# Kernel optimization log

Hardware: AMD Instinct MI355X
Metric: run time of the kernel (lower is better)

Reference implementation:

```python
import jax, jax.numpy as jnp
import numpy as np

B, S, E, H = 16, 256, 4096, 16
D = E // H  # 256; module's matmul pattern requires S == D and B == H


def setup_inputs() -> dict:
    rng = jax.random.key(0)
    k0, k1, k2, k3, k4 = jax.random.split(rng, 5)
    return {
        "query": jax.random.normal(k0, (B, S, E), jnp.float32),
        "key": jax.random.normal(k1, (B, S, E), jnp.float32),
        "value": jax.random.normal(k2, (B, S, E), jnp.float32),
        # out_proj: torch nn.Linear(E, E) -> y = x @ W.T + b
        "out_w": jax.random.normal(k3, (E, E), jnp.float32) * 0.02,
        "out_b": jnp.zeros((E,), jnp.float32),
    }


def reference(query, key, value, out_w, out_b):
    scale = D ** -0.5
    # split heads: [B, S, E] -> [B, H, S, D]
    q = (query * scale).reshape(B, S, H, D).transpose(0, 2, 1, 3)
    k = key.reshape(B, S, H, D).transpose(0, 2, 1, 3)
    v = value.reshape(B, S, H, D).transpose(0, 2, 1, 3)
    # torch.matmul(q_head, k_head) with NO transpose: contracts q's D with k's S
    # (valid because S == D). aw: [B, H, S, D]
    aw = jnp.einsum('bhit,bhtj->bhij', q, k)
    # attn_weights.transpose(0, 1): [B, H, ...] -> [H, B, ...]
    aw = jnp.swapaxes(aw, 0, 1)
    # eval mode path: softmax over last dim (no dropout)
    aw = jax.nn.softmax(aw, axis=-1)
    # torch.matmul(aw [H,B,S,D], v [B,H,S,D]): batch dims broadcast because B == H,
    # pairing elementwise -> out[x,y] = aw[x,y] @ v[x,y]
    out = jnp.einsum('xyit,xytj->xyij', aw, v)
    # transpose(1, 2) then reshape to (B, S, E)
    out = jnp.swapaxes(out, 1, 2).reshape(B, S, E)
    # out_proj
    return out @ out_w.T + out_b
```

## Files before the change

### kernel.cpp

```cpp
#include <hip/hip_runtime.h>

#define AS1 __attribute__((address_space(1)))
#define AS3 __attribute__((address_space(3)))

typedef __bf16 bf16x8 __attribute__((ext_vector_type(8)));
typedef float f32x4 __attribute__((ext_vector_type(4)));

__device__ __forceinline__ unsigned short f2bf(float f) {
  unsigned int u = __builtin_bit_cast(unsigned int, f);
  u += 0x7fffu + ((u >> 16) & 1u);
  return (unsigned short)(u >> 16);
}

__global__ __launch_bounds__(256) void kv_transpose(
    const float* __restrict__ key, const float* __restrict__ value,
    unsigned short* __restrict__ KT2, unsigned short* __restrict__ VT2) {
  __shared__ float tr[32 * 33];
  const int tid = threadIdx.x;
  const int ts  = blockIdx.y;
  const int pp  = blockIdx.x >> 3;
  const int s   = blockIdx.x & 7;
  const int b   = ts ? (pp >> 4) : (pp & 15);
  const int h   = ts ? (pp & 15) : (pp >> 4);
  const float* src = (ts ? value : key) + ((size_t)(b * 256 + s * 32)) * 4096 + h * 256;
  unsigned short* dst = (ts ? VT2 : KT2) + (size_t)(pp * 8 + s) * 8192;
  const int tt = tid >> 3;
  const int q8 = tid & 7;
  for (int jb = 0; jb < 8; ++jb) {
    float4 v = *(const float4*)(src + (size_t)tt * 4096 + jb * 32 + q8 * 4);
    tr[tt * 33 + q8 * 4 + 0] = v.x;
    tr[tt * 33 + q8 * 4 + 1] = v.y;
    tr[tt * 33 + q8 * 4 + 2] = v.z;
    tr[tt * 33 + q8 * 4 + 3] = v.w;
    __syncthreads();
    ushort4 o;
    o.x = f2bf(tr[(q8 * 4 + 0) * 33 + tt]);
    o.y = f2bf(tr[(q8 * 4 + 1) * 33 + tt]);
    o.z = f2bf(tr[(q8 * 4 + 2) * 33 + tt]);
    o.w = f2bf(tr[(q8 * 4 + 3) * 33 + tt]);
    *(ushort4*)(dst + (jb * 32 + tt) * 32 + q8 * 4) = o;
    __syncthreads();
  }
}

__global__ __launch_bounds__(256, 2) void attn_kernel(
    const float* __restrict__ qin, const unsigned short* __restrict__ KT2,
    const unsigned short* __restrict__ VT2, unsigned short* __restrict__ attn) {
  __shared__ __align__(16) unsigned short kv[8192];
  __shared__ __align__(16) unsigned short plds[4 * 16 * 264];

  const int tid  = threadIdx.x;
  const int lane = tid & 63;
  const int wave = tid >> 6;
  const int li   = lane & 15;
  const int ks   = lane >> 4;

  const int bid = blockIdx.x;
  const int pp  = (bid & 7) * 32 + ((bid >> 3) & 31);
  const int ib  = bid >> 8;
  const int x = pp >> 4, y = pp & 15;
  const int i0 = ib * 64 + wave * 16;

  bf16x8 qf[8];
  {
    const float* qrow = qin + ((size_t)(y * 256 + i0 + li)) * 4096 + x * 256 + ks * 8;
#pragma unroll
    for (int s = 0; s < 8; ++s) {
      float4 v0 = *(const float4*)(qrow + s * 32);
      float4 v1 = *(const float4*)(qrow + s * 32 + 4);
      union { bf16x8 v; unsigned short u[8]; } t;
      t.u[0] = f2bf(v0.x * 0.0625f); t.u[1] = f2bf(v0.y * 0.0625f);
      t.u[2] = f2bf(v0.z * 0.0625f); t.u[3] = f2bf(v0.w * 0.0625f);
      t.u[4] = f2bf(v1.x * 0.0625f); t.u[5] = f2bf(v1.y * 0.0625f);
      t.u[6] = f2bf(v1.z * 0.0625f); t.u[7] = f2bf(v1.w * 0.0625f);
      qf[s] = t.v;
    }
  }

  const f32x4 vzero = {0.f, 0.f, 0.f, 0.f};
  f32x4 sacc[16];
#pragma unroll
  for (int f = 0; f < 16; ++f) sacc[f] = vzero;

  const unsigned short* ktile = KT2 + (size_t)pp * 65536;
#pragma unroll
  for (int s = 0; s < 8; ++s) {
    __syncthreads();
#pragma unroll
    for (int cc = 0; cc < 4; ++cc) {
      const unsigned short* g = ktile + (size_t)s * 8192 + (cc * 256 + tid) * 8;
      __builtin_amdgcn_global_load_lds((AS1 unsigned int*)g,
          (AS3 unsigned int*)((AS3 char*)kv + cc * 4096 + wave * 1024), 16, 0, 0);
    }
    __syncthreads();
#pragma unroll
    for (int f = 0; f < 16; ++f) {
      bf16x8 bfr = *(const bf16x8*)&kv[(f * 16 + li) * 32 + ks * 8];
      sacc[f] = __builtin_amdgcn_mfma_f32_16x16x32_bf16(qf[s], bfr, sacc[f], 0, 0, 0);
    }
  }

  float sm[4];
#pragma unroll
  for (int qi = 0; qi < 4; ++qi) {
    float m = sacc[0][qi];
#pragma unroll
    for (int f = 1; f < 16; ++f) m = fmaxf(m, sacc[f][qi]);
    m = fmaxf(m, __shfl_xor(m, 1));
    m = fmaxf(m, __shfl_xor(m, 2));
    m = fmaxf(m, __shfl_xor(m, 4));
    m = fmaxf(m, __shfl_xor(m, 8));
    float ssum = 0.f;
#pragma unroll
    for (int f = 0; f < 16; ++f) {
      float pv = __expf(sacc[f][qi] - m);
      sacc[f][qi] = pv;
      ssum += pv;
    }
    ssum += __shfl_xor(ssum, 1);
    ssum += __shfl_xor(ssum, 2);
    ssum += __shfl_xor(ssum, 4);
    ssum += __shfl_xor(ssum, 8);
    sm[qi] = ssum;
  }

  unsigned short* pw = plds + wave * 4224;
#pragma unroll
  for (int f = 0; f < 16; ++f)
#pragma unroll
    for (int qi = 0; qi < 4; ++qi)
      pw[(ks * 4 + qi) * 264 + f * 16 + li] = f2bf(sacc[f][qi]);

  f32x4 oacc[16];
#pragma unroll
  for (int f = 0; f < 16; ++f) oacc[f] = vzero;
  const unsigned short* vtile = VT2 + (size_t)pp * 65536;
  const unsigned short* pr = plds + wave * 4224 + li * 264;
#pragma unroll
  for (int s2 = 0; s2 < 8; ++s2) {
    __syncthreads();
#pragma unroll
    for (int cc = 0; cc < 4; ++cc) {
      const unsigned short* g = vtile + (size_t)s2 * 8192 + (cc * 256 + tid) * 8;
      __builtin_amdgcn_global_load_lds((AS1 unsigned int*)g,
          (AS3 unsigned int*)((AS3 char*)kv + cc * 4096 + wave * 1024), 16, 0, 0);
    }
    __syncthreads();
    bf16x8 afr = *(const bf16x8*)&pr[s2 * 32 + ks * 8];
#pragma unroll
    for (int f = 0; f < 16; ++f) {
      bf16x8 bfr = *(const bf16x8*)&kv[(f * 16 + li) * 32 + ks * 8];
      oacc[f] = __builtin_amdgcn_mfma_f32_16x16x32_bf16(afr, bfr, oacc[f], 0, 0, 0);
    }
  }

  float rs4[4];
#pragma unroll
  for (int qi = 0; qi < 4; ++qi) rs4[qi] = 1.0f / sm[qi];
  unsigned short* abase = attn + (size_t)(x * 256 + i0 + ks * 4) * 4096 + y * 256 + li;
#pragma unroll
  for (int f = 0; f < 16; ++f)
#pragma unroll
    for (int qi = 0; qi < 4; ++qi)
      abase[(size_t)qi * 4096 + f * 16] = f2bf(oacc[f][qi] * rs4[qi]);
}

__global__ __launch_bounds__(256) void convw(const float* __restrict__ w,
                                             unsigned short* __restrict__ o) {
  const int i = blockIdx.x * 256 + threadIdx.x;
  const float4* s = (const float4*)w + (size_t)i * 2;
  float4 v0 = s[0], v1 = s[1];
  uint4 pk;
  pk.x = (unsigned)f2bf(v0.x) | ((unsigned)f2bf(v0.y) << 16);
  pk.y = (unsigned)f2bf(v0.z) | ((unsigned)f2bf(v0.w) << 16);
  pk.z = (unsigned)f2bf(v1.x) | ((unsigned)f2bf(v1.y) << 16);
  pk.w = (unsigned)f2bf(v1.z) | ((unsigned)f2bf(v1.w) << 16);
  *((uint4*)o + i) = pk;
}

__global__ __launch_bounds__(512, 2) void proj_gemm8(
    const unsigned short* __restrict__ A, const unsigned short* __restrict__ W,
    const float* __restrict__ bias, float* __restrict__ out) {
  __shared__ __align__(1024) char lds[131072];

  const int tid  = threadIdx.x;
  const int lane = tid & 63;
  const int w    = tid >> 6;
  const int li   = lane & 15;
  const int ks   = lane >> 4;
  const int wr   = w >> 2;
  const int wc   = w & 3;
  const int LB   = (li * 64 + ks * 16) ^ (((li >> 3) & 1) << 5);

  const int bid = blockIdx.x;
  const int swz = (bid & 7) * 32 + (bid >> 3);
  const int m0b = (swz >> 4) * 256, n0b = (swz & 15) * 256;

  unsigned sA[2], sB[2];
  int dstP[2];
#pragma unroll
  for (int j = 0; j < 2; ++j) {
    int P = j * 8192 + tid * 16;
    int L = P ^ (((P >> 9) & 1) << 5);
    int row = L >> 6, col = L & 63;
    dstP[j] = P;
    sA[j] = (unsigned)((m0b + row) * 8192 + col);
    sB[j] = (unsigned)((n0b + row) * 8192 + col);
  }
  const char* Ac = (const char*)A;
  const char* Wc = (const char*)W;
  AS3 char* L3 = (AS3 char*)lds;

  const f32x4 vzero = {0.f, 0.f, 0.f, 0.f};
  f32x4 acc[8][4];
#pragma unroll
  for (int m = 0; m < 8; ++m)
#pragma unroll
    for (int n = 0; n < 4; ++n) acc[m][n] = vzero;

#define STAGE(kt, slot) do {                                                   \
    const unsigned _ko = (unsigned)(kt) * 64u;                                 \
    const int _sl = (slot) * 32768;                                            \
    _Pragma("unroll") for (int j = 0; j < 2; ++j) {                            \
      __builtin_amdgcn_global_load_lds((AS1 unsigned int*)(Ac + sA[j] + _ko),  \
          (AS3 unsigned int*)(L3 + _sl + dstP[j]), 16, 0, 0);                  \
      __builtin_amdgcn_global_load_lds((AS1 unsigned int*)(Wc + sB[j] + _ko),  \
          (AS3 unsigned int*)(L3 + _sl + 16384 + dstP[j]), 16, 0, 0);          \
    } } while (0)
#define RD_A(S, M) (*(const bf16x8*)(lds + (S) + wr * 8192 + (M) * 1024 + LB))
#define RD_B(S, N) (*(const bf16x8*)(lds + (S) + 16384 + wc * 4096 + (N) * 1024 + LB))
#define MFMA(a, b, c) __builtin_amdgcn_mfma_f32_16x16x32_bf16((a), (b), (c), 0, 0, 0)

  STAGE(0, 0); STAGE(1, 1); STAGE(2, 2);
  asm volatile("s_waitcnt vmcnt(8)" ::: "memory");
  __builtin_amdgcn_s_barrier();

  for (int t = 0; t < 128; ++t) {
    const int sl = (t & 3) * 32768;
    bf16x8 af[8], bf[4];
    af[0] = RD_A(sl, 0);
#pragma unroll
    for (int n = 0; n < 4; ++n) bf[n] = RD_B(sl, n);
#pragma unroll
    for (int m = 1; m < 8; ++m) af[m] = RD_A(sl, m);

    const int kt = (t + 3 < 128) ? t + 3 : 127;
    STAGE(kt, (t + 3) & 3);

    __builtin_amdgcn_s_setprio(1);
#pragma unroll
    for (int m = 0; m < 8; ++m)
#pragma unroll
      for (int n = 0; n < 4; ++n)
        acc[m][n] = MFMA(af[m], bf[n], acc[m][n]);
    __builtin_amdgcn_s_setprio(0);

    asm volatile("s_waitcnt vmcnt(8)" ::: "memory");
    __builtin_amdgcn_s_barrier();
  }

  float bv[4];
#pragma unroll
  for (int n = 0; n < 4; ++n) bv[n] = bias[n0b + wc * 64 + n * 16 + li];
#pragma unroll
  for (int m = 0; m < 8; ++m) {
#pragma unroll
    for (int qi = 0; qi < 4; ++qi) {
      const int row = m0b + wr * 128 + m * 16 + ks * 4 + qi;
      float* orow = out + (size_t)row * 4096 + n0b + wc * 64 + li;
#pragma unroll
      for (int n = 0; n < 4; ++n) orow[n * 16] = acc[m][n][qi] + bv[n];
    }
  }
#undef STAGE
#undef RD_A
#undef RD_B
#undef MFMA
}

extern "C" void kernel_launch(void* const* d_in, const int* in_sizes, int n_in,
                              void* d_out, int out_size, void* d_ws, size_t ws_size,
                              hipStream_t stream) {
  const float* q = (const float*)d_in[0];
  const float* k = (const float*)d_in[1];
  const float* v = (const float*)d_in[2];
  const float* w = (const float*)d_in[3];
  const float* b = (const float*)d_in[4];
  float* out = (float*)d_out;
  char* ws = (char*)d_ws;

  unsigned short* attn = (unsigned short*)ws;
  unsigned short* KT2  = (unsigned short*)(ws + (size_t)33554432);
  unsigned short* VT2  = (unsigned short*)(ws + (size_t)67108864);
  unsigned short* wbf  = KT2;

  kv_transpose<<<dim3(2048, 2), 256, 0, stream>>>(k, v, KT2, VT2);
  attn_kernel<<<1024, 256, 0, stream>>>(q, KT2, VT2, attn);
  convw<<<8192, 256, 0, stream>>>(w, wbf);
  proj_gemm8<<<256, 512, 0, stream>>>(attn, wbf, b, out);
}
```

Baseline: 236.5 us.

## Halve projection GEMM block tile to 128x256 with triple-buffered LDS

The output projection GEMM moves from 256x256 tiles with 8 waves and 4-stage buffering to 128x256 tiles with 4 waves and 3-stage buffering, using 512 blocks instead of 256. Each block uses 72KB of LDS, which should let two blocks fit per CU and gives more blocks to spread across the 256 CUs. The cost is more global traffic per FLOP, since the A/B reuse per tile is lower, and a shallower prefetch pipeline.

```diff
diff --git a/kernel.cpp b/kernel.cpp
--- a/kernel.cpp
+++ b/kernel.cpp
@@ -178,33 +178,39 @@
   *((uint4*)o + i) = pk;
 }
 
-__global__ __launch_bounds__(512, 2) void proj_gemm8(
+__global__ __launch_bounds__(256, 2) void proj_gemm2(
     const unsigned short* __restrict__ A, const unsigned short* __restrict__ W,
     const float* __restrict__ bias, float* __restrict__ out) {
-  __shared__ __align__(1024) char lds[131072];
+  __shared__ __align__(1024) char lds[73728];
 
   const int tid  = threadIdx.x;
   const int lane = tid & 63;
-  const int w    = tid >> 6;
+  const int wc   = tid >> 6;
   const int li   = lane & 15;
   const int ks   = lane >> 4;
-  const int wr   = w >> 2;
-  const int wc   = w & 3;
   const int LB   = (li * 64 + ks * 16) ^ (((li >> 3) & 1) << 5);
 
   const int bid = blockIdx.x;
-  const int swz = (bid & 7) * 32 + (bid >> 3);
-  const int m0b = (swz >> 4) * 256, n0b = (swz & 15) * 256;
-
-  unsigned sA[2], sB[2];
-  int dstP[2];
+  const int swz = (bid & 7) * 64 + (bid >> 3);
+  const int mi  = swz >> 4, ni = swz & 15;
+  const int m0b = mi * 128, n0b = ni * 256;
+
+  unsigned sA[2], sB[4];
+  int dPA[2], dPB[4];
 #pragma unroll
   for (int j = 0; j < 2; ++j) {
-    int P = j * 8192 + tid * 16;
+    int P = j * 4096 + tid * 16;
     int L = P ^ (((P >> 9) & 1) << 5);
     int row = L >> 6, col = L & 63;
-    dstP[j] = P;
+    dPA[j] = P;
     sA[j] = (unsigned)((m0b + row) * 8192 + col);
+  }
+#pragma unroll
+  for (int j = 0; j < 4; ++j) {
+    int P = j * 4096 + tid * 16;
+    int L = P ^ (((P >> 9) & 1) << 5);
+    int row = L >> 6, col = L & 63;
+    dPB[j] = P;
     sB[j] = (unsigned)((n0b + row) * 8192 + col);
   }
   const char* Ac = (const char*)A;
@@ -220,32 +226,32 @@
 
 #define STAGE(kt, slot) do {                                                   \
     const unsigned _ko = (unsigned)(kt) * 64u;                                 \
-    const int _sl = (slot) * 32768;                                            \
-    _Pragma("unroll") for (int j = 0; j < 2; ++j) {                            \
+    _Pragma("unroll") for (int j = 0; j < 2; ++j)                              \
       __builtin_amdgcn_global_load_lds((AS1 unsigned int*)(Ac + sA[j] + _ko),  \
-          (AS3 unsigned int*)(L3 + _sl + dstP[j]), 16, 0, 0);                  \
+          (AS3 unsigned int*)(L3 + (slot) + dPA[j]), 16, 0, 0);                \
+    _Pragma("unroll") for (int j = 0; j < 4; ++j)                              \
       __builtin_amdgcn_global_load_lds((AS1 unsigned int*)(Wc + sB[j] + _ko),  \
-          (AS3 unsigned int*)(L3 + _sl + 16384 + dstP[j]), 16, 0, 0);          \
-    } } while (0)
-#define RD_A(S, M) (*(const bf16x8*)(lds + (S) + wr * 8192 + (M) * 1024 + LB))
-#define RD_B(S, N) (*(const bf16x8*)(lds + (S) + 16384 + wc * 4096 + (N) * 1024 + LB))
+          (AS3 unsigned int*)(L3 + (slot) + 8192 + dPB[j]), 16, 0, 0);         \
+  } while (0)
+#define RD_A(S, M) (*(const bf16x8*)(lds + (S) + (M) * 1024 + LB))
+#define RD_B(S, N) (*(const bf16x8*)(lds + (S) + 8192 + wc * 4096 + (N) * 1024 + LB))
 #define MFMA(a, b, c) __builtin_amdgcn_mfma_f32_16x16x32_bf16((a), (b), (c), 0, 0, 0)
 
-  STAGE(0, 0); STAGE(1, 1); STAGE(2, 2);
-  asm volatile("s_waitcnt vmcnt(8)" ::: "memory");
+  STAGE(0, 0); STAGE(1, 24576);
+  asm volatile("s_waitcnt vmcnt(6)" ::: "memory");
   __builtin_amdgcn_s_barrier();
 
+  int rs = 0, wslot = 49152;
   for (int t = 0; t < 128; ++t) {
-    const int sl = (t & 3) * 32768;
     bf16x8 af[8], bf[4];
-    af[0] = RD_A(sl, 0);
-#pragma unroll
-    for (int n = 0; n < 4; ++n) bf[n] = RD_B(sl, n);
-#pragma unroll
-    for (int m = 1; m < 8; ++m) af[m] = RD_A(sl, m);
-
-    const int kt = (t + 3 < 128) ? t + 3 : 127;
-    STAGE(kt, (t + 3) & 3);
+    af[0] = RD_A(rs, 0);
+#pragma unroll
+    for (int n = 0; n < 4; ++n) bf[n] = RD_B(rs, n);
+#pragma unroll
+    for (int m = 1; m < 8; ++m) af[m] = RD_A(rs, m);
+
+    const int kt = (t + 2 < 128) ? t + 2 : 127;
+    STAGE(kt, wslot);
 
     __builtin_amdgcn_s_setprio(1);
 #pragma unroll
@@ -255,8 +261,10 @@
         acc[m][n] = MFMA(af[m], bf[n], acc[m][n]);
     __builtin_amdgcn_s_setprio(0);
 
-    asm volatile("s_waitcnt vmcnt(8)" ::: "memory");
+    asm volatile("s_waitcnt vmcnt(6)" ::: "memory");
     __builtin_amdgcn_s_barrier();
+    rs = (rs == 49152) ? 0 : rs + 24576;
+    wslot = (wslot == 49152) ? 0 : wslot + 24576;
   }
 
   float bv[4];
@@ -266,7 +274,7 @@
   for (int m = 0; m < 8; ++m) {
 #pragma unroll
     for (int qi = 0; qi < 4; ++qi) {
-      const int row = m0b + wr * 128 + m * 16 + ks * 4 + qi;
+      const int row = m0b + m * 16 + ks * 4 + qi;
       float* orow = out + (size_t)row * 4096 + n0b + wc * 64 + li;
 #pragma unroll
       for (int n = 0; n < 4; ++n) orow[n * 16] = acc[m][n][qi] + bv[n];
@@ -297,5 +305,5 @@
   kv_transpose<<<dim3(2048, 2), 256, 0, stream>>>(k, v, KT2, VT2);
   attn_kernel<<<1024, 256, 0, stream>>>(q, KT2, VT2, attn);
   convw<<<8192, 256, 0, stream>>>(w, wbf);
-  proj_gemm8<<<256, 512, 0, stream>>>(attn, wbf, b, out);
-}
+  proj_gemm2<<<512, 256, 0, stream>>>(attn, wbf, b, out);
+}
```

Result: slower. 255.3 us (+7.9%).

## Load GEMM A operand directly into registers, stage only W through LDS

Applied to the files above, without the earlier changes.

The projection GEMM now reads its A-fragments straight from global memory into registers, double-buffered one k-step ahead, instead of staging A through LDS. Only the W tile goes through a 3-slot LDS ring, so LDS drops from 128KB to 48KB. The block-to-tile mapping is also changed so each group of 8 blocks shares two M rows across N tiles. This aims to cut LDS traffic and footprint, but global loads now sit closer to use with a shallower prefetch, which can expose memory latency, and it raises register pressure.

```diff
diff --git a/kernel.cpp b/kernel.cpp
--- a/kernel.cpp
+++ b/kernel.cpp
@@ -178,10 +178,10 @@
   *((uint4*)o + i) = pk;
 }
 
-__global__ __launch_bounds__(512, 2) void proj_gemm8(
+__global__ __launch_bounds__(512, 2) void proj_gemm_ag(
     const unsigned short* __restrict__ A, const unsigned short* __restrict__ W,
     const float* __restrict__ bias, float* __restrict__ out) {
-  __shared__ __align__(1024) char lds[131072];
+  __shared__ __align__(1024) char lds[49152];
 
   const int tid  = threadIdx.x;
   const int lane = tid & 63;
@@ -193,24 +193,27 @@
   const int LB   = (li * 64 + ks * 16) ^ (((li >> 3) & 1) << 5);
 
   const int bid = blockIdx.x;
-  const int swz = (bid & 7) * 32 + (bid >> 3);
-  const int m0b = (swz >> 4) * 256, n0b = (swz & 15) * 256;
-
-  unsigned sA[2], sB[2];
-  int dstP[2];
-#pragma unroll
-  for (int j = 0; j < 2; ++j) {
-    int P = j * 8192 + tid * 16;
+  const int x8  = bid & 7, jj = bid >> 3;
+  const int mi  = 2 * x8 + (jj >> 4);
+  const int ni  = jj & 15;
+  const int m0b = mi * 256, n0b = ni * 256;
+
+  unsigned sB[2];
+  int dPB[2];
+#pragma unroll
+  for (int j2 = 0; j2 < 2; ++j2) {
+    int P = j2 * 8192 + tid * 16;
     int L = P ^ (((P >> 9) & 1) << 5);
     int row = L >> 6, col = L & 63;
-    dstP[j] = P;
-    sA[j] = (unsigned)((m0b + row) * 8192 + col);
-    sB[j] = (unsigned)((n0b + row) * 8192 + col);
+    dPB[j2] = P;
+    sB[j2] = (unsigned)((n0b + row) * 8192 + col);
   }
   const char* Ac = (const char*)A;
   const char* Wc = (const char*)W;
   AS3 char* L3 = (AS3 char*)lds;
 
+  const size_t aRow = (size_t)(m0b + wr * 128 + li) * 8192 + (size_t)ks * 16;
+
   const f32x4 vzero = {0.f, 0.f, 0.f, 0.f};
   f32x4 acc[8][4];
 #pragma unroll
@@ -218,45 +221,48 @@
 #pragma unroll
     for (int n = 0; n < 4; ++n) acc[m][n] = vzero;
 
-#define STAGE(kt, slot) do {                                                   \
-    const unsigned _ko = (unsigned)(kt) * 64u;                                 \
-    const int _sl = (slot) * 32768;                                            \
-    _Pragma("unroll") for (int j = 0; j < 2; ++j) {                            \
-      __builtin_amdgcn_global_load_lds((AS1 unsigned int*)(Ac + sA[j] + _ko),  \
-          (AS3 unsigned int*)(L3 + _sl + dstP[j]), 16, 0, 0);                  \
-      __builtin_amdgcn_global_load_lds((AS1 unsigned int*)(Wc + sB[j] + _ko),  \
-          (AS3 unsigned int*)(L3 + _sl + 16384 + dstP[j]), 16, 0, 0);          \
-    } } while (0)
-#define RD_A(S, M) (*(const bf16x8*)(lds + (S) + wr * 8192 + (M) * 1024 + LB))
-#define RD_B(S, N) (*(const bf16x8*)(lds + (S) + 16384 + wc * 4096 + (N) * 1024 + LB))
+#define PREF(T, DST) do {                                                      \
+    _Pragma("unroll") for (int m = 0; m < 8; ++m)                              \
+      DST[m] = *(const bf16x8*)(Ac + aRow + (size_t)m * 131072 +               \
+                                (unsigned)(T) * 64u);                          \
+  } while (0)
+#define STB(T, SL) do {                                                        \
+    const unsigned _ko = (unsigned)(T) * 64u;                                  \
+    _Pragma("unroll") for (int j2 = 0; j2 < 2; ++j2)                           \
+      __builtin_amdgcn_global_load_lds((AS1 unsigned int*)(Wc + sB[j2] + _ko), \
+          (AS3 unsigned int*)(L3 + (SL) + dPB[j2]), 16, 0, 0);                 \
+  } while (0)
 #define MFMA(a, b, c) __builtin_amdgcn_mfma_f32_16x16x32_bf16((a), (b), (c), 0, 0, 0)
 
-  STAGE(0, 0); STAGE(1, 1); STAGE(2, 2);
-  asm volatile("s_waitcnt vmcnt(8)" ::: "memory");
+  bf16x8 aA[8], aB[8];
+
+  STB(0, 0); STB(1, 16384);
+  PREF(0, aA);
+  asm volatile("s_waitcnt vmcnt(0)" ::: "memory");
   __builtin_amdgcn_s_barrier();
 
-  for (int t = 0; t < 128; ++t) {
-    const int sl = (t & 3) * 32768;
-    bf16x8 af[8], bf[4];
-    af[0] = RD_A(sl, 0);
-#pragma unroll
-    for (int n = 0; n < 4; ++n) bf[n] = RD_B(sl, n);
-#pragma unroll
-    for (int m = 1; m < 8; ++m) af[m] = RD_A(sl, m);
-
-    const int kt = (t + 3 < 128) ? t + 3 : 127;
-    STAGE(kt, (t + 3) & 3);
-
-    __builtin_amdgcn_s_setprio(1);
-#pragma unroll
-    for (int m = 0; m < 8; ++m)
-#pragma unroll
-      for (int n = 0; n < 4; ++n)
-        acc[m][n] = MFMA(af[m], bf[n], acc[m][n]);
-    __builtin_amdgcn_s_setprio(0);
-
-    asm volatile("s_waitcnt vmcnt(8)" ::: "memory");
-    __builtin_amdgcn_s_barrier();
+  int rs = 0, ws = 32768;
+
+#define TILE(T, AC, AN) do {                                                   \
+    bf16x8 bf[4];                                                              \
+    _Pragma("unroll") for (int n = 0; n < 4; ++n)                              \
+      bf[n] = *(const bf16x8*)(lds + rs + wc * 4096 + n * 1024 + LB);          \
+    PREF(((T) + 1 < 128) ? (T) + 1 : 127, AN);                                 \
+    STB(((T) + 2 < 128) ? (T) + 2 : 127, ws);                                  \
+    __builtin_amdgcn_s_setprio(1);                                             \
+    _Pragma("unroll") for (int m = 0; m < 8; ++m)                              \
+      _Pragma("unroll") for (int n = 0; n < 4; ++n)                            \
+        acc[m][n] = MFMA(AC[m], bf[n], acc[m][n]);                             \
+    __builtin_amdgcn_s_setprio(0);                                             \
+    asm volatile("s_waitcnt vmcnt(2)" ::: "memory");                           \
+    __builtin_amdgcn_s_barrier();                                              \
+    rs = (rs == 32768) ? 0 : rs + 16384;                                       \
+    ws = (ws == 32768) ? 0 : ws + 16384;                                       \
+  } while (0)
+
+  for (int tt = 0; tt < 64; ++tt) {
+    TILE(2 * tt,     aA, aB);
+    TILE(2 * tt + 1, aB, aA);
   }
 
   float bv[4];
@@ -272,10 +278,10 @@
       for (int n = 0; n < 4; ++n) orow[n * 16] = acc[m][n][qi] + bv[n];
     }
   }
-#undef STAGE
-#undef RD_A
-#undef RD_B
+#undef PREF
+#undef STB
 #undef MFMA
+#undef TILE
 }
 
 extern "C" void kernel_launch(void* const* d_in, const int* in_sizes, int n_in,
@@ -297,5 +303,5 @@
   kv_transpose<<<dim3(2048, 2), 256, 0, stream>>>(k, v, KT2, VT2);
   attn_kernel<<<1024, 256, 0, stream>>>(q, KT2, VT2, attn);
   convw<<<8192, 256, 0, stream>>>(w, wbf);
-  proj_gemm8<<<256, 512, 0, stream>>>(attn, wbf, b, out);
-}
+  proj_gemm_ag<<<256, 512, 0, stream>>>(attn, wbf, b, out);
+}
```

Measured after the change: 411.8 us. 1.74x slower.

## Restructure projection GEMM into double-buffered K=128 stages with split loads

Applied to the files above, without the earlier changes.

The output projection GEMM moves from a 4-slot ring of K=64 tiles with prefetch depth 3 to a double buffer holding K=128 per stage. Each iteration runs two K=64 MFMA sub-steps, and the A and B loads for the next stage are issued between them. The aim is to halve the number of barriers and loop iterations while keeping loads overlapped with compute. The cost is a shallower prefetch distance and a full vmcnt(0) wait every iteration, which can expose global memory latency.

```diff
diff --git a/kernel.cpp b/kernel.cpp
--- a/kernel.cpp
+++ b/kernel.cpp
@@ -178,7 +178,7 @@
   *((uint4*)o + i) = pk;
 }
 
-__global__ __launch_bounds__(512, 2) void proj_gemm8(
+__global__ __launch_bounds__(512, 2) void proj_gemm64(
     const unsigned short* __restrict__ A, const unsigned short* __restrict__ W,
     const float* __restrict__ bias, float* __restrict__ out) {
   __shared__ __align__(1024) char lds[131072];
@@ -218,35 +218,41 @@
 #pragma unroll
     for (int n = 0; n < 4; ++n) acc[m][n] = vzero;
 
-#define STAGE(kt, slot) do {                                                   \
-    const unsigned _ko = (unsigned)(kt) * 64u;                                 \
-    const int _sl = (slot) * 32768;                                            \
-    _Pragma("unroll") for (int j = 0; j < 2; ++j) {                            \
-      __builtin_amdgcn_global_load_lds((AS1 unsigned int*)(Ac + sA[j] + _ko),  \
-          (AS3 unsigned int*)(L3 + _sl + dstP[j]), 16, 0, 0);                  \
-      __builtin_amdgcn_global_load_lds((AS1 unsigned int*)(Wc + sB[j] + _ko),  \
-          (AS3 unsigned int*)(L3 + _sl + 16384 + dstP[j]), 16, 0, 0);          \
-    } } while (0)
-#define RD_A(S, M) (*(const bf16x8*)(lds + (S) + wr * 8192 + (M) * 1024 + LB))
-#define RD_B(S, N) (*(const bf16x8*)(lds + (S) + 16384 + wc * 4096 + (N) * 1024 + LB))
+#define STG_A(kt, buf, kk) do {                                                \
+    const unsigned _o = (unsigned)(kt) * 128u + (unsigned)(kk) * 64u;          \
+    _Pragma("unroll") for (int j = 0; j < 2; ++j)                              \
+      __builtin_amdgcn_global_load_lds((AS1 unsigned int*)(Ac + sA[j] + _o),   \
+          (AS3 unsigned int*)(L3 + (buf) + (kk) * 16384 + dstP[j]), 16, 0, 0); \
+  } while (0)
+#define STG_B(kt, buf, kk) do {                                                \
+    const unsigned _o = (unsigned)(kt) * 128u + (unsigned)(kk) * 64u;          \
+    _Pragma("unroll") for (int j = 0; j < 2; ++j)                              \
+      __builtin_amdgcn_global_load_lds((AS1 unsigned int*)(Wc + sB[j] + _o),   \
+          (AS3 unsigned int*)(L3 + (buf) + 32768 + (kk) * 16384 + dstP[j]),    \
+          16, 0, 0);                                                           \
+  } while (0)
+#define RD_A(buf, kk, m) (*(const bf16x8*)(lds + (buf) + (kk) * 16384 +        \
+                                           wr * 8192 + (m) * 1024 + LB))
+#define RD_B(buf, kk, n) (*(const bf16x8*)(lds + (buf) + 32768 + (kk) * 16384 + \
+                                           wc * 4096 + (n) * 1024 + LB))
 #define MFMA(a, b, c) __builtin_amdgcn_mfma_f32_16x16x32_bf16((a), (b), (c), 0, 0, 0)
 
-  STAGE(0, 0); STAGE(1, 1); STAGE(2, 2);
-  asm volatile("s_waitcnt vmcnt(8)" ::: "memory");
+  STG_A(0, 0, 0); STG_A(0, 0, 1); STG_B(0, 0, 0); STG_B(0, 0, 1);
+  asm volatile("s_waitcnt vmcnt(0)" ::: "memory");
   __builtin_amdgcn_s_barrier();
 
-  for (int t = 0; t < 128; ++t) {
-    const int sl = (t & 3) * 32768;
+  for (int t = 0; t < 64; ++t) {
+    const int cur = (t & 1) * 65536;
+    const int oth = 65536 - cur;
+    const int k1  = (t < 63) ? t + 1 : 63;
     bf16x8 af[8], bf[4];
-    af[0] = RD_A(sl, 0);
-#pragma unroll
-    for (int n = 0; n < 4; ++n) bf[n] = RD_B(sl, n);
-#pragma unroll
-    for (int m = 1; m < 8; ++m) af[m] = RD_A(sl, m);
-
-    const int kt = (t + 3 < 128) ? t + 3 : 127;
-    STAGE(kt, (t + 3) & 3);
-
+
+    STG_A(k1, oth, 0); STG_A(k1, oth, 1);
+    af[0] = RD_A(cur, 0, 0);
+#pragma unroll
+    for (int n = 0; n < 4; ++n) bf[n] = RD_B(cur, 0, n);
+#pragma unroll
+    for (int m = 1; m < 8; ++m) af[m] = RD_A(cur, 0, m);
     __builtin_amdgcn_s_setprio(1);
 #pragma unroll
     for (int m = 0; m < 8; ++m)
@@ -255,7 +261,21 @@
         acc[m][n] = MFMA(af[m], bf[n], acc[m][n]);
     __builtin_amdgcn_s_setprio(0);
 
-    asm volatile("s_waitcnt vmcnt(8)" ::: "memory");
+    STG_B(k1, oth, 0); STG_B(k1, oth, 1);
+    af[0] = RD_A(cur, 1, 0);
+#pragma unroll
+    for (int n = 0; n < 4; ++n) bf[n] = RD_B(cur, 1, n);
+#pragma unroll
+    for (int m = 1; m < 8; ++m) af[m] = RD_A(cur, 1, m);
+    __builtin_amdgcn_s_setprio(1);
+#pragma unroll
+    for (int m = 0; m < 8; ++m)
+#pragma unroll
+      for (int n = 0; n < 4; ++n)
+        acc[m][n] = MFMA(af[m], bf[n], acc[m][n]);
+    __builtin_amdgcn_s_setprio(0);
+
+    asm volatile("s_waitcnt vmcnt(0)" ::: "memory");
     __builtin_amdgcn_s_barrier();
   }
 
@@ -272,7 +292,8 @@
       for (int n = 0; n < 4; ++n) orow[n * 16] = acc[m][n][qi] + bv[n];
     }
   }
-#undef STAGE
+#undef STG_A
+#undef STG_B
 #undef RD_A
 #undef RD_B
 #undef MFMA
@@ -297,5 +318,5 @@
   kv_transpose<<<dim3(2048, 2), 256, 0, stream>>>(k, v, KT2, VT2);
   attn_kernel<<<1024, 256, 0, stream>>>(q, KT2, VT2, attn);
   convw<<<8192, 256, 0, stream>>>(w, wbf);
-  proj_gemm8<<<256, 512, 0, stream>>>(attn, wbf, b, out);
-}
+  proj_gemm64<<<256, 512, 0, stream>>>(attn, wbf, b, out);
+}
```

New measurement: 230.3 us. -2.6%, faster.
